# Optimization experiments

Hardware: AMD Instinct MI355X
Metric: run time of the kernel (lower is better)

## Reference

```python
import jax, jax.numpy as jnp
import numpy as np

G, KP, EPS = 4, 9, 1e-5  # deformable groups, 3x3 kernel points, BN eps


def setup_inputs() -> dict:
    key = jax.random.key(0)
    ks = jax.random.split(key, 16)
    N, C1, C2, H, W = 8, 256, 256, 64, 64
    c = int(C1 * 1.0) // 16 * 16  # 256 internal width
    OM = int(np.ceil(G * KP * 3 / 8) * 8)  # 112 padded offset/mask dim (108 used)
    sd = 0.02
    return {
        "x": jax.random.normal(ks[0], (N, C1, H, W), jnp.float32),
        "cv1_w": jax.random.normal(ks[1], (c, C1), jnp.float32) * sd,
        "cv1_b": jax.random.normal(ks[2], (c,), jnp.float32) * sd,
        "value_w": jax.random.normal(ks[3], (c, c), jnp.float32) * sd,
        "value_b": jax.random.normal(ks[4], (c,), jnp.float32) * sd,
        "dw_w": jax.random.normal(ks[5], (c,), jnp.float32) * sd + 1.0,
        "dw_b": jax.random.normal(ks[6], (c,), jnp.float32) * sd,
        "om_w": jax.random.normal(ks[7], (OM, c), jnp.float32) * sd,
        "om_b": jax.random.normal(ks[8], (OM,), jnp.float32) * sd,
        "out_w": jax.random.normal(ks[9], (c, c), jnp.float32) * sd,
        "cv2_w": jax.random.normal(ks[10], (C2, c), jnp.float32) * sd,
        "bn_gamma": jnp.ones((C2,), jnp.float32),
        "bn_beta": jnp.zeros((C2,), jnp.float32),
        "bn_mean": jax.random.normal(ks[11], (C2,), jnp.float32) * 0.1,
        "bn_var": jax.random.uniform(ks[12], (C2,), jnp.float32, minval=0.5, maxval=1.5),
    }


def _dcnv4(value, offset_mask, H, W):
    """DCNv4 core: offset-based bilinear sampling + unnormalized-mask aggregation.
    value: (N,H,W,c) NHWC features; offset_mask: (N,H,W,OM), per group layout
    [2*KP offsets (dx,dy pairs), KP masks]; no softmax on masks (DCNv4)."""
    N, c = value.shape[0], value.shape[-1]
    GC = c // G
    om = offset_mask[..., : G * KP * 3].reshape(N, H, W, G, 3 * KP)
    offs = om[..., : 2 * KP].reshape(N, H, W, G, KP, 2)  # (dx, dy), x = width axis
    mask = om[..., 2 * KP:]                               # (N,H,W,G,KP)
    ky, kx = jnp.meshgrid(jnp.arange(-1, 2, dtype=jnp.float32),
                          jnp.arange(-1, 2, dtype=jnp.float32), indexing="ij")
    kx, ky = kx.reshape(KP), ky.reshape(KP)               # 3x3 dilation-1 grid
    base_x = jnp.arange(W, dtype=jnp.float32)[None, None, :, None, None]
    base_y = jnp.arange(H, dtype=jnp.float32)[None, :, None, None, None]
    px = base_x + kx + offs[..., 0]                       # (N,H,W,G,KP) abs pixel x
    py = base_y + ky + offs[..., 1]
    x0, y0 = jnp.floor(px), jnp.floor(py)
    fx, fy = px - x0, py - y0
    x0i, y0i = x0.astype(jnp.int32), y0.astype(jnp.int32)
    vflat = value.reshape(N, H * W, G, GC).transpose(0, 2, 1, 3)  # (N,G,L,GC)
    acc = jnp.zeros((N, G, H, W, KP, GC), value.dtype)
    for dy, dx, wgt in ((0, 0, (1 - fy) * (1 - fx)), (0, 1, (1 - fy) * fx),
                        (1, 0, fy * (1 - fx)), (1, 1, fy * fx)):
        yy, xx = y0i + dy, x0i + dx
        valid = (yy >= 0) & (yy < H) & (xx >= 0) & (xx < W)   # zero padding
        idx = jnp.clip(yy, 0, H - 1) * W + jnp.clip(xx, 0, W - 1)
        idx_g = idx.transpose(0, 3, 1, 2, 4).reshape(N, G, H * W * KP)
        smp = jnp.take_along_axis(vflat, idx_g[..., None], axis=2)
        smp = smp.reshape(N, G, H, W, KP, GC)
        acc = acc + smp * (wgt * valid).transpose(0, 3, 1, 2, 4)[..., None]
    out = (acc * mask.transpose(0, 3, 1, 2, 4)[..., None]).sum(axis=4)  # (N,G,H,W,GC)
    return out.transpose(0, 2, 3, 1, 4).reshape(N, H, W, c)


def reference(x, cv1_w, cv1_b, value_w, value_b, dw_w, dw_b, om_w, om_b,
              out_w, cv2_w, bn_gamma, bn_beta, bn_mean, bn_var):
    N, C1, H, W = x.shape
    t = jnp.einsum("nchw,dc->nhwd", x, cv1_w) + cv1_b       # cv1 1x1 conv -> NHWC
    value = t @ value_w.T + value_b                          # DCNv4 value_proj
    om = (t * dw_w + dw_b) @ om_w.T + om_b                   # depthwise 1x1 + linear
    y = _dcnv4(value, om, H, W)
    y = y @ out_w.T                                          # output_proj (no bias)
    y = jnp.einsum("nhwc,dc->nhwd", y, cv2_w)                # cv2 1x1 (no bias)
    y = (y - bn_mean) * bn_gamma * jax.lax.rsqrt(bn_var + EPS) + bn_beta  # BN (eval)
    y = y * jax.nn.sigmoid(y)                                # SiLU
    return y.transpose(0, 3, 1, 2)                           # back to NCHW
```

## Files before the change

### kernel.cpp

```cpp
#include <hip/hip_runtime.h>
#include <hip/hip_bf16.h>
#include <math.h>

#define NN    8
#define HH    64
#define WW    64
#define HW    4096
#define NHW   32768
#define EPSBN 1e-5f

#define PCELLS   4624
#define PELEMS   295936
#define ROWS68   4352

typedef __attribute__((ext_vector_type(8))) short short8v;
typedef __attribute__((ext_vector_type(4))) float f32x4;
typedef __attribute__((ext_vector_type(2))) float f32x2;

__device__ __forceinline__ float b2f(unsigned short u) {
    union { unsigned int i; float f; } v; v.i = ((unsigned int)u) << 16; return v.f;
}
__device__ __forceinline__ unsigned short f2b(float f) {
    __hip_bfloat16 h = __float2bfloat16(f);
    return *reinterpret_cast<const unsigned short*>(&h);
}
__device__ __forceinline__ f32x2 bf2x(int u) {
    union { int i; float f; } a, b;
    a.i = u << 16;
    b.i = u & 0xffff0000;
    f32x2 r; r[0] = a.f; r[1] = b.f; return r;
}


__global__ __launch_bounds__(256)
void prep_kernel(const float* __restrict__ cv1_w, const float* __restrict__ cv1_b,
                 const float* __restrict__ value_w, const float* __restrict__ value_b,
                 const float* __restrict__ dw_w, const float* __restrict__ dw_b,
                 const float* __restrict__ om_w, const float* __restrict__ om_b,
                 const float* __restrict__ out_w, const float* __restrict__ cv2_w,
                 const float* __restrict__ bn_g, const float* __restrict__ bn_b,
                 const float* __restrict__ bn_m, const float* __restrict__ bn_v,
                 unsigned short* __restrict__ Wallbf, float* __restrict__ ball,
                 unsigned short* __restrict__ Woutbf, float* __restrict__ bout)
{
    int job = blockIdx.x * 256 + threadIdx.x;
    if (job < 65536) {
        int d = job >> 8, cc = job & 255;
        float s0=0.f, s1=0.f, s2=0.f, s3=0.f;
        for (int e = 0; e < 256; e += 4) {
            float4 wv = *reinterpret_cast<const float4*>(&value_w[d*256+e]);
            s0 = fmaf(wv.x, cv1_w[(e+0)*256+cc], s0);
            s1 = fmaf(wv.y, cv1_w[(e+1)*256+cc], s1);
            s2 = fmaf(wv.z, cv1_w[(e+2)*256+cc], s2);
            s3 = fmaf(wv.w, cv1_w[(e+3)*256+cc], s3);
        }
        Wallbf[job] = f2b((s0+s1)+(s2+s3));
    } else if (job < 94208) {
        int idx = job - 65536;
        int o = idx >> 8, cc = idx & 255;
        float s0=0.f, s1=0.f, s2=0.f, s3=0.f;
        for (int e = 0; e < 256; e += 4) {
            float4 wv = *reinterpret_cast<const float4*>(&om_w[o*256+e]);
            float4 dv = *reinterpret_cast<const float4*>(&dw_w[e]);
            s0 = fmaf(wv.x*dv.x, cv1_w[(e+0)*256+cc], s0);
            s1 = fmaf(wv.y*dv.y, cv1_w[(e+1)*256+cc], s1);
            s2 = fmaf(wv.z*dv.z, cv1_w[(e+2)*256+cc], s2);
            s3 = fmaf(wv.w*dv.w, cv1_w[(e+3)*256+cc], s3);
        }
        Wallbf[job] = f2b((s0+s1)+(s2+s3));
    } else if (job < 98304) {
        Wallbf[job] = 0;
    } else if (job < 163840) {
        int idx = job - 98304;
        int d = idx >> 8, cc = idx & 255;
        float s0=0.f, s1=0.f, s2=0.f, s3=0.f;
        for (int e = 0; e < 256; e += 4) {
            float4 wv = *reinterpret_cast<const float4*>(&cv2_w[d*256+e]);
            s0 = fmaf(wv.x, out_w[(e+0)*256+cc], s0);
            s1 = fmaf(wv.y, out_w[(e+1)*256+cc], s1);
            s2 = fmaf(wv.z, out_w[(e+2)*256+cc], s2);
            s3 = fmaf(wv.w, out_w[(e+3)*256+cc], s3);
        }
        float sc = bn_g[d] * rsqrtf(bn_v[d] + EPSBN);
        Woutbf[idx] = f2b(((s0+s1)+(s2+s3)) * sc);
    } else if (job < 164096) {
        int d = job - 163840;
        float s = value_b[d];
        for (int e = 0; e < 256; ++e) s = fmaf(value_w[d*256+e], cv1_b[e], s);
        ball[d] = s;
    } else if (job < 164208) {
        int o = job - 164096;
        float s = om_b[o];
        for (int e = 0; e < 256; ++e)
            s = fmaf(om_w[o*256+e], fmaf(dw_w[e], cv1_b[e], dw_b[e]), s);
        ball[256 + o] = s;
    } else if (job < 164224) {
        ball[368 + job - 164208] = 0.f;
    } else if (job < 164480) {
        int d = job - 164224;
        float sc = bn_g[d] * rsqrtf(bn_v[d] + EPSBN);
        bout[d] = fmaf(-bn_m[d], sc, bn_b[d]);
    }
}

__global__ __launch_bounds__(256)
void zero_pad_kernel(unsigned short* __restrict__ V2)
{
    int bid = blockIdx.x;
    unsigned short* base = V2 + (size_t)(bid >> 3) * PELEMS;
    int off = (bid & 7) * 528;
    int t = threadIdx.x;
    for (int ii = t; ii < 528; ii += 256) {
        int idx = off + ii;
        int cellsub = idx >> 3;
        int chunk = idx & 7;
        int cell;
        if (cellsub < 272) {
            int r = cellsub / 68;
            int c = cellsub - r * 68;
            int row = (r < 2) ? r : r + 62;
            cell = row * 68 + c;
        } else {
            int i2 = cellsub - 272;
            int row = 2 + (i2 >> 2);
            int cs = i2 & 3;
            int col = (cs < 2) ? cs : cs + 62;
            cell = row * 68 + col;
        }
        *reinterpret_cast<int4*>(&base[cell * 64 + chunk * 8]) = int4{0,0,0,0};
    }
}

__global__ __launch_bounds__(256)
void gemm_vo_kernel(const float* __restrict__ x, const unsigned short* __restrict__ Wallbf,
                    const float* __restrict__ ball,
                    unsigned short* __restrict__ V2, unsigned short* __restrict__ OM)
{
    __shared__ unsigned short As[8192];
    __shared__ unsigned short Bs[8192];
    int t = threadIdx.x;
    int m0 = blockIdx.y * 128;
    int n0 = blockIdx.x * 128;
    int nimg = m0 >> 12, hw0 = m0 & 4095;
    int lane = t & 63;
    int wv = t >> 6;
    int wr = wv >> 1, wc = wv & 1;
    int r_l = lane & 15, kg_l = lane >> 4;
    int ci = t >> 6;
    int l  = t & 63;

    const float* xbase = x + (size_t)(nimg * 256) * 4096 + hw0;

    f32x4 acc[4][4] = {};

    for (int kt = 0; kt < 4; ++kt) {
        int c0 = kt * 64;
        float2 val[16];
        #pragma unroll
        for (int i = 0; i < 16; ++i)
            val[i] = *reinterpret_cast<const float2*>(
                &xbase[(size_t)(c0 + ci*16 + i) * 4096 + 2*l]);
        __syncthreads();
        #pragma unroll
        for (int rsel = 0; rsel < 2; ++rsel) {
            int row = 2*l + rsel;
            #pragma unroll
            for (int kgi = 0; kgi < 2; ++kgi) {
                int kg = ci*2 + kgi;
                short8v s;
                #pragma unroll
                for (int j = 0; j < 8; ++j)
                    s[j] = (short)f2b(rsel ? val[kgi*8+j].y : val[kgi*8+j].x);
                *reinterpret_cast<short8v*>(&As[row*64 + ((kg ^ (row & 7)) << 3)]) = s;
            }
        }
        #pragma unroll
        for (int i = 0; i < 4; ++i) {
            int idx = t + i*256;
            int row = idx >> 3, kg = idx & 7;
            *reinterpret_cast<short8v*>(&Bs[row*64 + ((kg ^ (row & 7)) << 3)]) =
                *reinterpret_cast<const short8v*>(&Wallbf[(size_t)(n0 + row)*256 + c0 + kg*8]);
        }
        __syncthreads();
        #pragma unroll
        for (int ks = 0; ks < 2; ++ks) {
            short8v af[4], bfr[4];
            #pragma unroll
            for (int m = 0; m < 4; ++m) {
                int row = wr*64 + m*16 + r_l;
                af[m] = *reinterpret_cast<const short8v*>(
                    &As[row*64 + (((ks*4 + kg_l) ^ (row & 7)) << 3)]);
            }
            #pragma unroll
            for (int n = 0; n < 4; ++n) {
                int row = wc*64 + n*16 + r_l;
                bfr[n] = *reinterpret_cast<const short8v*>(
                    &Bs[row*64 + (((ks*4 + kg_l) ^ (row & 7)) << 3)]);
            }
            #pragma unroll
            for (int m = 0; m < 4; ++m)
                #pragma unroll
                for (int n = 0; n < 4; ++n)
                    acc[m][n] = __builtin_amdgcn_mfma_f32_16x16x32_bf16(af[m], bfr[n], acc[m][n], 0, 0, 0);
        }
    }

    #pragma unroll
    for (int n = 0; n < 4; ++n) {
        int d = n0 + wc*64 + n*16 + r_l;
        float bb = ball[d];
        #pragma unroll
        for (int m = 0; m < 4; ++m) {
            int pr = m0 + wr*64 + m*16 + (kg_l << 2);
            #pragma unroll
            for (int r = 0; r < 4; ++r) {
                float res = acc[m][n][r] + bb;
                int p = pr + r;
                if (d < 256) {
                    int g = d >> 6, ch = d & 63;
                    int hw = p & 4095;
                    int yy = hw >> 6, xx = hw & 63;
                    size_t cell = (size_t)((p >> 12)*4 + g) * PCELLS + (yy + 2)*68 + (xx + 2);
                    V2[cell * 64 + ch] = f2b(res);
                } else if (d < 368) {
                    OM[(size_t)p * 112 + (d - 256)] = f2b(res);
                }
            }
        }
    }
}

__device__ __forceinline__
void gemm_mainloop(const unsigned short* __restrict__ A, const unsigned short* __restrict__ B,
                   int m0, int n0, unsigned short* As, unsigned short* Bs,
                   f32x4 (&acc)[4][4], int t)
{
    int lane = t & 63;
    int wv = t >> 6;
    int wr = wv >> 1, wc = wv & 1;
    int r_l = lane & 15;
    int kg_l = lane >> 4;

    for (int kt = 0; kt < 4; ++kt) {
        int c0 = kt * 64;
        #pragma unroll
        for (int i = 0; i < 4; ++i) {
            int idx = t + i * 256;
            int kg = idx & 7, row = idx >> 3;
            int soff = row*64 + ((kg ^ (row & 7)) << 3);
            *reinterpret_cast<short8v*>(&As[soff]) =
                *reinterpret_cast<const short8v*>(&A[(size_t)(m0 + row)*256 + c0 + kg*8]);
            *reinterpret_cast<short8v*>(&Bs[soff]) =
                *reinterpret_cast<const short8v*>(&B[(size_t)(n0 + row)*256 + c0 + kg*8]);
        }
        __syncthreads();
        #pragma unroll
        for (int ks = 0; ks < 2; ++ks) {
            short8v af[4], bfr[4];
            #pragma unroll
            for (int m = 0; m < 4; ++m) {
                int row = wr*64 + m*16 + r_l;
                af[m] = *reinterpret_cast<const short8v*>(
                    &As[row*64 + (((ks*4 + kg_l) ^ (row & 7)) << 3)]);
            }
            #pragma unroll
            for (int n = 0; n < 4; ++n) {
                int row = wc*64 + n*16 + r_l;
                bfr[n] = *reinterpret_cast<const short8v*>(
                    &Bs[row*64 + (((ks*4 + kg_l) ^ (row & 7)) << 3)]);
            }
            #pragma unroll
            for (int m = 0; m < 4; ++m)
                #pragma unroll
                for (int n = 0; n < 4; ++n)
                    acc[m][n] = __builtin_amdgcn_mfma_f32_16x16x32_bf16(af[m], bfr[n], acc[m][n], 0, 0, 0);
        }
        __syncthreads();
    }
}

__global__ __launch_bounds__(256)
void gemm_out_kernel(const unsigned short* __restrict__ Woutbf, const unsigned short* __restrict__ y,
                     const float* __restrict__ bout, float* __restrict__ out)
{
    __shared__ unsigned short lds[2 * 8192];
    int t = threadIdx.x;
    int m0 = blockIdx.x * 128;
    int n0 = blockIdx.y * 128;
    f32x4 acc[4][4] = {};
    gemm_mainloop(Woutbf, y, m0, n0, lds, lds + 8192, acc, t);

    int lane = t & 63;
    int wv = t >> 6, wr = wv >> 1, wc = wv & 1;
    int r_l = lane & 15, kg_l = lane >> 4;
    int nimg = n0 >> 12;
    int hwb = n0 & 4095;
    #pragma unroll
    for (int m = 0; m < 4; ++m) {
        int dbase = m0 + wr*64 + m*16 + (kg_l << 2);
        #pragma unroll
        for (int r = 0; r < 4; ++r) {
            int d = dbase + r;
            float bb = bout[d];
            #pragma unroll
            for (int n = 0; n < 4; ++n) {
                int pcol = wc*64 + n*16 + r_l;
                float z = acc[m][n][r] + bb;
                float sv = z / (1.f + __expf(-z));
                out[((size_t)(nimg*256 + d))*4096 + hwb + pcol] = sv;
            }
        }
    }
}

__global__ __launch_bounds__(256)
void dcn_kernel(const unsigned short* __restrict__ V2, const unsigned short* __restrict__ OM,
                unsigned short* __restrict__ y)
{
    __shared__ float om_s[8][108];
    int t = threadIdx.x;
    int bid = blockIdx.x;
    int logical = ((bid & 7) << 9) + (bid >> 3);
    int p0 = logical * 8;

    for (int i = t; i < 864; i += 256) {
        int pl = i / 108, j = i - pl * 108;
        om_s[pl][j] = b2f(OM[(size_t)(p0 + pl)*112 + j]);
    }
    __syncthreads();

    int slot = t >> 3, ch8 = t & 7;
    int pl = slot >> 2, g = slot & 3;
    int p = p0 + pl;
    int hw = p & 4095;
    int h = hw >> 6, w = hw & 63;
    const unsigned short* plane =
        V2 + (size_t)((p >> 12)*4 + g) * PELEMS + ch8*8;
    const float* o = &om_s[pl][g*27];

    f32x2 acc2[4] = {};
    #pragma unroll
    for (int k = 0; k < 9; ++k) {
        float dxo = o[2*k], dyo = o[2*k+1], m = o[18+k];
        float px = fminf(fmaxf((float)(w + (k % 3) - 1) + dxo, -1.f), 64.f);
        float py = fminf(fmaxf((float)(h + (k / 3) - 1) + dyo, -1.f), 64.f);
        float x0f = floorf(px), y0f = floorf(py);
        float fx = px - x0f, fy = py - y0f;
        float gx = 1.f - fx, gy = 1.f - fy;
        int cell = ((int)y0f + 2) * 68 + ((int)x0f + 2);
        const unsigned short* cp0 = plane + cell * 64;
        const unsigned short* cp1 = cp0 + ROWS68;
        int4 v00 = *reinterpret_cast<const int4*>(cp0);
        int4 v01 = *reinterpret_cast<const int4*>(cp0 + 64);
        int4 v10 = *reinterpret_cast<const int4*>(cp1);
        int4 v11 = *reinterpret_cast<const int4*>(cp1 + 64);
        float gym = gy * m, fym = fy * m;
        float w00 = gym*gx, w01 = gym*fx, w10 = fym*gx, w11 = fym*fx;
        {
            f32x2 W; W[0] = w00; W[1] = w00;
            int a[4] = {v00.x, v00.y, v00.z, v00.w};
            #pragma unroll
            for (int q = 0; q < 4; ++q) acc2[q] += bf2x(a[q]) * W;
        }
        {
            f32x2 W; W[0] = w01; W[1] = w01;
            int a[4] = {v01.x, v01.y, v01.z, v01.w};
            #pragma unroll
            for (int q = 0; q < 4; ++q) acc2[q] += bf2x(a[q]) * W;
        }
        {
            f32x2 W; W[0] = w10; W[1] = w10;
            int a[4] = {v10.x, v10.y, v10.z, v10.w};
            #pragma unroll
            for (int q = 0; q < 4; ++q) acc2[q] += bf2x(a[q]) * W;
        }
        {
            f32x2 W; W[0] = w11; W[1] = w11;
            int a[4] = {v11.x, v11.y, v11.z, v11.w};
            #pragma unroll
            for (int q = 0; q < 4; ++q) acc2[q] += bf2x(a[q]) * W;
        }
    }

    short8v ov;
    #pragma unroll
    for (int q = 0; q < 4; ++q) {
        ov[2*q]   = (short)f2b(acc2[q][0]);
        ov[2*q+1] = (short)f2b(acc2[q][1]);
    }
    *reinterpret_cast<short8v*>(&y[(size_t)p*256 + g*64 + ch8*8]) = ov;
}

extern "C" void kernel_launch(void* const* d_in, const int* in_sizes, int n_in,
                              void* d_out, int out_size, void* d_ws, size_t ws_size,
                              hipStream_t stream) {
    const float* x       = (const float*)d_in[0];
    const float* cv1_w   = (const float*)d_in[1];
    const float* cv1_b   = (const float*)d_in[2];
    const float* value_w = (const float*)d_in[3];
    const float* value_b = (const float*)d_in[4];
    const float* dw_w    = (const float*)d_in[5];
    const float* dw_b    = (const float*)d_in[6];
    const float* om_w    = (const float*)d_in[7];
    const float* om_b    = (const float*)d_in[8];
    const float* out_w   = (const float*)d_in[9];
    const float* cv2_w   = (const float*)d_in[10];
    const float* bn_g    = (const float*)d_in[11];
    const float* bn_b    = (const float*)d_in[12];
    const float* bn_m    = (const float*)d_in[13];
    const float* bn_v    = (const float*)d_in[14];

    char* ws = (char*)d_ws;
    unsigned short* V2     = (unsigned short*)(ws);
    unsigned short* OM     = (unsigned short*)(ws + 18939904);
    unsigned short* y      = (unsigned short*)(ws + 26279936);
    unsigned short* Wallbf = (unsigned short*)(ws + 43057152);
    unsigned short* Woutbf = (unsigned short*)(ws + 43253760);
    float*          ball   = (float*)(ws + 43384832);
    float*          bout   = (float*)(ws + 43386368);
    float* out = (float*)d_out;

    prep_kernel<<<643, 256, 0, stream>>>(cv1_w, cv1_b, value_w, value_b, dw_w, dw_b,
                                         om_w, om_b, out_w, cv2_w,
                                         bn_g, bn_b, bn_m, bn_v,
                                         Wallbf, ball, Woutbf, bout);
    zero_pad_kernel<<<256, 256, 0, stream>>>(V2);
    gemm_vo_kernel<<<dim3(3, 256), 256, 0, stream>>>(x, Wallbf, ball, V2, OM);
    dcn_kernel<<<4096, 256, 0, stream>>>(V2, OM, y);
    gemm_out_kernel<<<dim3(2, 256), 256, 0, stream>>>(Woutbf, y, bout, out);
}
```

Measured before the change: 93.52 us.

## Fuse weight prep with pad zeroing, tile prep GEMMs, widen DCN per-thread channels

Weight-folding products now run as shared-memory tiled 64x64 GEMMs in a few blocks instead of one thread per output element. Pad zeroing of the value planes is merged into the same prep launch, which removes one kernel launch. The deformable sampling kernel now has each thread handle 16 channels over 16 pixels per block, halving the grid and amortizing offset math and shared-memory loads. The cost is more registers per thread, fewer blocks to hide latency in the gather kernel, and a prep step that runs on only 40 blocks.

```diff
diff --git a/kernel.cpp b/kernel.cpp
--- a/kernel.cpp
+++ b/kernel.cpp
@@ -33,101 +33,129 @@
 
 
 __global__ __launch_bounds__(256)
-void prep_kernel(const float* __restrict__ cv1_w, const float* __restrict__ cv1_b,
-                 const float* __restrict__ value_w, const float* __restrict__ value_b,
-                 const float* __restrict__ dw_w, const float* __restrict__ dw_b,
-                 const float* __restrict__ om_w, const float* __restrict__ om_b,
-                 const float* __restrict__ out_w, const float* __restrict__ cv2_w,
-                 const float* __restrict__ bn_g, const float* __restrict__ bn_b,
-                 const float* __restrict__ bn_m, const float* __restrict__ bn_v,
-                 unsigned short* __restrict__ Wallbf, float* __restrict__ ball,
-                 unsigned short* __restrict__ Woutbf, float* __restrict__ bout)
+void prep_all_kernel(const float* __restrict__ cv1_w, const float* __restrict__ cv1_b,
+                     const float* __restrict__ value_w, const float* __restrict__ value_b,
+                     const float* __restrict__ dw_w, const float* __restrict__ dw_b,
+                     const float* __restrict__ om_w, const float* __restrict__ om_b,
+                     const float* __restrict__ out_w, const float* __restrict__ cv2_w,
+                     const float* __restrict__ bn_g, const float* __restrict__ bn_b,
+                     const float* __restrict__ bn_m, const float* __restrict__ bn_v,
+                     unsigned short* __restrict__ Wallbf, float* __restrict__ ball,
+                     unsigned short* __restrict__ Woutbf, float* __restrict__ bout,
+                     unsigned short* __restrict__ V2)
 {
-    int job = blockIdx.x * 256 + threadIdx.x;
-    if (job < 65536) {
-        int d = job >> 8, cc = job & 255;
-        float s0=0.f, s1=0.f, s2=0.f, s3=0.f;
-        for (int e = 0; e < 256; e += 4) {
-            float4 wv = *reinterpret_cast<const float4*>(&value_w[d*256+e]);
-            s0 = fmaf(wv.x, cv1_w[(e+0)*256+cc], s0);
-            s1 = fmaf(wv.y, cv1_w[(e+1)*256+cc], s1);
-            s2 = fmaf(wv.z, cv1_w[(e+2)*256+cc], s2);
-            s3 = fmaf(wv.w, cv1_w[(e+3)*256+cc], s3);
-        }
-        Wallbf[job] = f2b((s0+s1)+(s2+s3));
-    } else if (job < 94208) {
-        int idx = job - 65536;
-        int o = idx >> 8, cc = idx & 255;
-        float s0=0.f, s1=0.f, s2=0.f, s3=0.f;
-        for (int e = 0; e < 256; e += 4) {
-            float4 wv = *reinterpret_cast<const float4*>(&om_w[o*256+e]);
-            float4 dv = *reinterpret_cast<const float4*>(&dw_w[e]);
-            s0 = fmaf(wv.x*dv.x, cv1_w[(e+0)*256+cc], s0);
-            s1 = fmaf(wv.y*dv.y, cv1_w[(e+1)*256+cc], s1);
-            s2 = fmaf(wv.z*dv.z, cv1_w[(e+2)*256+cc], s2);
-            s3 = fmaf(wv.w*dv.w, cv1_w[(e+3)*256+cc], s3);
-        }
-        Wallbf[job] = f2b((s0+s1)+(s2+s3));
-    } else if (job < 98304) {
-        Wallbf[job] = 0;
-    } else if (job < 163840) {
-        int idx = job - 98304;
-        int d = idx >> 8, cc = idx & 255;
-        float s0=0.f, s1=0.f, s2=0.f, s3=0.f;
-        for (int e = 0; e < 256; e += 4) {
-            float4 wv = *reinterpret_cast<const float4*>(&cv2_w[d*256+e]);
-            s0 = fmaf(wv.x, out_w[(e+0)*256+cc], s0);
-            s1 = fmaf(wv.y, out_w[(e+1)*256+cc], s1);
-            s2 = fmaf(wv.z, out_w[(e+2)*256+cc], s2);
-            s3 = fmaf(wv.w, out_w[(e+3)*256+cc], s3);
-        }
-        float sc = bn_g[d] * rsqrtf(bn_v[d] + EPSBN);
-        Woutbf[idx] = f2b(((s0+s1)+(s2+s3)) * sc);
-    } else if (job < 164096) {
-        int d = job - 163840;
+    int bid = blockIdx.x;
+    int t = threadIdx.x;
+
+    if (bid < 40) {
+        __shared__ float As[16][64];
+        __shared__ float Bs[16][64];
+        int kind, m0, n0;
+        if (bid < 16)      { kind = 0; m0 = (bid >> 2) * 64;        n0 = (bid & 3) * 64; }
+        else if (bid < 24) { kind = 1; m0 = ((bid - 16) >> 2) * 64; n0 = ((bid - 16) & 3) * 64; }
+        else               { kind = 2; m0 = ((bid - 24) >> 2) * 64; n0 = ((bid - 24) & 3) * 64; }
+
+        const float* A = (kind == 0) ? value_w : (kind == 1) ? om_w : cv2_w;
+        const float* B = (kind == 2) ? out_w : cv1_w;
+
+        int am = t >> 2, ak4 = (t & 3) * 4;
+        int bk = t >> 4, bn4 = (t & 15) * 4;
+
+        float acc[4][4] = {};
+        int px = (t & 15) << 2;
+        int dx = (t >> 4) << 2;
+
+        for (int c0 = 0; c0 < 256; c0 += 16) {
+            float4 av;
+            if (kind == 1 && (m0 + am) >= 112) {
+                av = float4{0.f, 0.f, 0.f, 0.f};
+            } else {
+                av = *reinterpret_cast<const float4*>(&A[(size_t)(m0 + am) * 256 + c0 + ak4]);
+                if (kind == 1) {
+                    float4 dv = *reinterpret_cast<const float4*>(&dw_w[c0 + ak4]);
+                    av.x *= dv.x; av.y *= dv.y; av.z *= dv.z; av.w *= dv.w;
+                }
+            }
+            As[ak4 + 0][am] = av.x;
+            As[ak4 + 1][am] = av.y;
+            As[ak4 + 2][am] = av.z;
+            As[ak4 + 3][am] = av.w;
+            *reinterpret_cast<float4*>(&Bs[bk][bn4]) =
+                *reinterpret_cast<const float4*>(&B[(size_t)(c0 + bk) * 256 + n0 + bn4]);
+            __syncthreads();
+            #pragma unroll
+            for (int k = 0; k < 16; ++k) {
+                float4 a = *reinterpret_cast<const float4*>(&As[k][px]);
+                float4 b = *reinterpret_cast<const float4*>(&Bs[k][dx]);
+                float avv[4] = {a.x, a.y, a.z, a.w};
+                float bvv[4] = {b.x, b.y, b.z, b.w};
+                #pragma unroll
+                for (int i = 0; i < 4; ++i)
+                    #pragma unroll
+                    for (int j = 0; j < 4; ++j)
+                        acc[i][j] = fmaf(avv[i], bvv[j], acc[i][j]);
+            }
+            __syncthreads();
+        }
+
+        #pragma unroll
+        for (int i = 0; i < 4; ++i) {
+            int m = m0 + px + i;
+            if (kind == 1 && m >= 112) continue;
+            float sc = 1.f;
+            if (kind == 2) sc = bn_g[m] * rsqrtf(bn_v[m] + EPSBN);
+            #pragma unroll
+            for (int j = 0; j < 4; ++j) {
+                float v = acc[i][j] * sc;
+                int cc = n0 + dx + j;
+                if (kind == 0)      Wallbf[m * 256 + cc] = f2b(v);
+                else if (kind == 1) Wallbf[(256 + m) * 256 + cc] = f2b(v);
+                else                Woutbf[m * 256 + cc] = f2b(v);
+            }
+        }
+    } else if (bid == 40) {
+        int d = t;
         float s = value_b[d];
         for (int e = 0; e < 256; ++e) s = fmaf(value_w[d*256+e], cv1_b[e], s);
         ball[d] = s;
-    } else if (job < 164208) {
-        int o = job - 164096;
-        float s = om_b[o];
-        for (int e = 0; e < 256; ++e)
-            s = fmaf(om_w[o*256+e], fmaf(dw_w[e], cv1_b[e], dw_b[e]), s);
-        ball[256 + o] = s;
-    } else if (job < 164224) {
-        ball[368 + job - 164208] = 0.f;
-    } else if (job < 164480) {
-        int d = job - 164224;
-        float sc = bn_g[d] * rsqrtf(bn_v[d] + EPSBN);
-        bout[d] = fmaf(-bn_m[d], sc, bn_b[d]);
-    }
-}
-
-__global__ __launch_bounds__(256)
-void zero_pad_kernel(unsigned short* __restrict__ V2)
-{
-    int bid = blockIdx.x;
-    unsigned short* base = V2 + (size_t)(bid >> 3) * PELEMS;
-    int off = (bid & 7) * 528;
-    int t = threadIdx.x;
-    for (int ii = t; ii < 528; ii += 256) {
-        int idx = off + ii;
-        int cellsub = idx >> 3;
-        int chunk = idx & 7;
-        int cell;
-        if (cellsub < 272) {
-            int r = cellsub / 68;
-            int c = cellsub - r * 68;
-            int row = (r < 2) ? r : r + 62;
-            cell = row * 68 + c;
-        } else {
-            int i2 = cellsub - 272;
-            int row = 2 + (i2 >> 2);
-            int cs = i2 & 3;
-            int col = (cs < 2) ? cs : cs + 62;
-            cell = row * 68 + col;
-        }
-        *reinterpret_cast<int4*>(&base[cell * 64 + chunk * 8]) = int4{0,0,0,0};
+    } else if (bid == 41) {
+        if (t < 112) {
+            float s = om_b[t];
+            for (int e = 0; e < 256; ++e)
+                s = fmaf(om_w[t*256+e], fmaf(dw_w[e], cv1_b[e], dw_b[e]), s);
+            ball[256 + t] = s;
+        } else if (t < 128) {
+            ball[256 + t] = 0.f;
+        }
+        short8v z = {};
+        *reinterpret_cast<short8v*>(&Wallbf[368*256 + t*16]) = z;
+        *reinterpret_cast<short8v*>(&Wallbf[368*256 + t*16 + 8]) = z;
+    } else if (bid == 42) {
+        float sc = bn_g[t] * rsqrtf(bn_v[t] + EPSBN);
+        bout[t] = fmaf(-bn_m[t], sc, bn_b[t]);
+    } else {
+        int pb = bid - 43;
+        unsigned short* base = V2 + (size_t)(pb >> 3) * PELEMS;
+        int off = (pb & 7) * 528;
+        for (int ii = t; ii < 528; ii += 256) {
+            int idx = off + ii;
+            int cellsub = idx >> 3;
+            int chunk = idx & 7;
+            int cell;
+            if (cellsub < 272) {
+                int r = cellsub / 68;
+                int c = cellsub - r * 68;
+                int row = (r < 2) ? r : r + 62;
+                cell = row * 68 + c;
+            } else {
+                int i2 = cellsub - 272;
+                int row = 2 + (i2 >> 2);
+                int cs = i2 & 3;
+                int col = (cs < 2) ? cs : cs + 62;
+                cell = row * 68 + col;
+            }
+            *reinterpret_cast<int4*>(&base[cell * 64 + chunk * 8]) = int4{0,0,0,0};
+        }
     }
 }
 
@@ -317,28 +345,28 @@
 void dcn_kernel(const unsigned short* __restrict__ V2, const unsigned short* __restrict__ OM,
                 unsigned short* __restrict__ y)
 {
-    __shared__ float om_s[8][108];
+    __shared__ float om_s[16][108];
     int t = threadIdx.x;
     int bid = blockIdx.x;
-    int logical = ((bid & 7) << 9) + (bid >> 3);
-    int p0 = logical * 8;
-
-    for (int i = t; i < 864; i += 256) {
+    int logical = ((bid & 7) << 8) + (bid >> 3);
+    int p0 = logical * 16;
+
+    for (int i = t; i < 1728; i += 256) {
         int pl = i / 108, j = i - pl * 108;
         om_s[pl][j] = b2f(OM[(size_t)(p0 + pl)*112 + j]);
     }
     __syncthreads();
 
-    int slot = t >> 3, ch8 = t & 7;
+    int slot = t >> 2, ch16 = t & 3;
     int pl = slot >> 2, g = slot & 3;
     int p = p0 + pl;
     int hw = p & 4095;
     int h = hw >> 6, w = hw & 63;
     const unsigned short* plane =
-        V2 + (size_t)((p >> 12)*4 + g) * PELEMS + ch8*8;
+        V2 + (size_t)((p >> 12)*4 + g) * PELEMS + ch16*16;
     const float* o = &om_s[pl][g*27];
 
-    f32x2 acc2[4] = {};
+    f32x2 acc2[8] = {};
     #pragma unroll
     for (int k = 0; k < 9; ++k) {
         float dxo = o[2*k], dyo = o[2*k+1], m = o[18+k];
@@ -350,45 +378,41 @@
         int cell = ((int)y0f + 2) * 68 + ((int)x0f + 2);
         const unsigned short* cp0 = plane + cell * 64;
         const unsigned short* cp1 = cp0 + ROWS68;
-        int4 v00 = *reinterpret_cast<const int4*>(cp0);
-        int4 v01 = *reinterpret_cast<const int4*>(cp0 + 64);
-        int4 v10 = *reinterpret_cast<const int4*>(cp1);
-        int4 v11 = *reinterpret_cast<const int4*>(cp1 + 64);
+        int4 va[4], vb[4];
+        va[0] = *reinterpret_cast<const int4*>(cp0);
+        vb[0] = *reinterpret_cast<const int4*>(cp0 + 8);
+        va[1] = *reinterpret_cast<const int4*>(cp0 + 64);
+        vb[1] = *reinterpret_cast<const int4*>(cp0 + 72);
+        va[2] = *reinterpret_cast<const int4*>(cp1);
+        vb[2] = *reinterpret_cast<const int4*>(cp1 + 8);
+        va[3] = *reinterpret_cast<const int4*>(cp1 + 64);
+        vb[3] = *reinterpret_cast<const int4*>(cp1 + 72);
         float gym = gy * m, fym = fy * m;
-        float w00 = gym*gx, w01 = gym*fx, w10 = fym*gx, w11 = fym*fx;
-        {
-            f32x2 W; W[0] = w00; W[1] = w00;
-            int a[4] = {v00.x, v00.y, v00.z, v00.w};
-            #pragma unroll
-            for (int q = 0; q < 4; ++q) acc2[q] += bf2x(a[q]) * W;
-        }
-        {
-            f32x2 W; W[0] = w01; W[1] = w01;
-            int a[4] = {v01.x, v01.y, v01.z, v01.w};
-            #pragma unroll
-            for (int q = 0; q < 4; ++q) acc2[q] += bf2x(a[q]) * W;
-        }
-        {
-            f32x2 W; W[0] = w10; W[1] = w10;
-            int a[4] = {v10.x, v10.y, v10.z, v10.w};
-            #pragma unroll
-            for (int q = 0; q < 4; ++q) acc2[q] += bf2x(a[q]) * W;
-        }
-        {
-            f32x2 W; W[0] = w11; W[1] = w11;
-            int a[4] = {v11.x, v11.y, v11.z, v11.w};
-            #pragma unroll
-            for (int q = 0; q < 4; ++q) acc2[q] += bf2x(a[q]) * W;
-        }
-    }
-
-    short8v ov;
+        float wt[4] = {gym*gx, gym*fx, fym*gx, fym*fx};
+        #pragma unroll
+        for (int c = 0; c < 4; ++c) {
+            f32x2 W; W[0] = wt[c]; W[1] = wt[c];
+            int a[4] = {va[c].x, va[c].y, va[c].z, va[c].w};
+            int b[4] = {vb[c].x, vb[c].y, vb[c].z, vb[c].w};
+            #pragma unroll
+            for (int q = 0; q < 4; ++q) {
+                acc2[q]     += bf2x(a[q]) * W;
+                acc2[4 + q] += bf2x(b[q]) * W;
+            }
+        }
+    }
+
+    unsigned short* yp = &y[(size_t)p*256 + g*64 + ch16*16];
+    short8v ov0, ov1;
     #pragma unroll
     for (int q = 0; q < 4; ++q) {
-        ov[2*q]   = (short)f2b(acc2[q][0]);
-        ov[2*q+1] = (short)f2b(acc2[q][1]);
-    }
-    *reinterpret_cast<short8v*>(&y[(size_t)p*256 + g*64 + ch8*8]) = ov;
+        ov0[2*q]   = (short)f2b(acc2[q][0]);
+        ov0[2*q+1] = (short)f2b(acc2[q][1]);
+        ov1[2*q]   = (short)f2b(acc2[4+q][0]);
+        ov1[2*q+1] = (short)f2b(acc2[4+q][1]);
+    }
+    *reinterpret_cast<short8v*>(yp) = ov0;
+    *reinterpret_cast<short8v*>(yp + 8) = ov1;
 }
 
 extern "C" void kernel_launch(void* const* d_in, const int* in_sizes, int n_in,
@@ -420,12 +444,11 @@
     float*          bout   = (float*)(ws + 43386368);
     float* out = (float*)d_out;
 
-    prep_kernel<<<643, 256, 0, stream>>>(cv1_w, cv1_b, value_w, value_b, dw_w, dw_b,
-                                         om_w, om_b, out_w, cv2_w,
-                                         bn_g, bn_b, bn_m, bn_v,
-                                         Wallbf, ball, Woutbf, bout);
-    zero_pad_kernel<<<256, 256, 0, stream>>>(V2);
+    prep_all_kernel<<<299, 256, 0, stream>>>(cv1_w, cv1_b, value_w, value_b, dw_w, dw_b,
+                                             om_w, om_b, out_w, cv2_w,
+                                             bn_g, bn_b, bn_m, bn_v,
+                                             Wallbf, ball, Woutbf, bout, V2);
     gemm_vo_kernel<<<dim3(3, 256), 256, 0, stream>>>(x, Wallbf, ball, V2, OM);
-    dcn_kernel<<<4096, 256, 0, stream>>>(V2, OM, y);
+    dcn_kernel<<<2048, 256, 0, stream>>>(V2, OM, y);
     gemm_out_kernel<<<dim3(2, 256), 256, 0, stream>>>(Woutbf, y, bout, out);
 }
```

Result: slower. 101.1 us (+8.2%).
